# Kernel tuning notes

Measured on AMD Instinct MI355X. Metric: run time of the kernel, lower is better.

The kernel has to match this reference:

```python
import jax, jax.numpy as jnp
import numpy as np

N = 1_000_000
H, W = 480, 640
MIN_DEPTH, MAX_DEPTH = 0.0, 30.0


def setup_inputs() -> dict:
    key = jax.random.key(0)
    k1, k2, k3 = jax.random.split(key, 3)
    scale = jnp.array([W - 1, H - 1], dtype=jnp.float32)
    mkpts0_f = jax.random.uniform(k1, (N, 2), dtype=jnp.float32) * scale
    mkpts1_f = jax.random.uniform(k2, (N, 2), dtype=jnp.float32) * scale
    mconf = jax.random.uniform(k3, (N,), dtype=jnp.float32)
    K = jnp.array([[520.0, 0.0, 320.0],
                   [0.0, 520.0, 240.0],
                   [0.0, 0.0, 1.0]], dtype=jnp.float32)
    K0 = K[None]  # [1,3,3]
    K1 = K[None]
    c, s = float(np.cos(0.1)), float(np.sin(0.1))
    T_0to1 = jnp.array([[c, 0.0, s, 0.2],
                        [0.0, 1.0, 0.0, 0.0],
                        [-s, 0.0, c, 0.05],
                        [0.0, 0.0, 0.0, 1.0]], dtype=jnp.float32)[None]  # [1,4,4]
    image0 = jnp.zeros((1, 1, H, W), dtype=jnp.float32)
    m_bids = jnp.zeros((N,), dtype=jnp.int32)  # single batch element
    return {"T_0to1": T_0to1, "K0": K0, "K1": K1, "mconf": mconf,
            "mkpts0_f": mkpts0_f, "mkpts1_f": mkpts1_f,
            "image0": image0, "m_bids": m_bids}


def _triangulate(T_0to1, K0, K1, mconf, kpts0, kpts1):
    # Projection matrices: P0 = K0 @ [I|0], P1 = K1 @ T[:3,:]
    proj_identity = jnp.eye(3, 4, dtype=K0.dtype)
    P0 = K0[0] @ proj_identity          # [3,4]
    P1 = K1[0] @ T_0to1[0, :3, :]       # [3,4]
    P = jnp.stack([P0, P1], axis=0)     # [V=2,3,4]

    pts = jnp.stack([kpts0, kpts1], axis=1)              # [N,2,2]
    conf = jnp.stack([jnp.ones_like(mconf), mconf], 1)   # [N,2] (self conf = 1)

    # A[n,v] = pts[n,v,:,None] * P[v,2,None,:] - P[v,:2]   -> [N,V,2,4]
    A = pts[..., None] * P[None, :, 2, None, :] - P[None, :, :2, :]
    A = A * conf[:, :, None, None]
    A = A.reshape(A.shape[0], 4, 4)                       # [N,4,4]

    # torch.svd returns V with A = U S V^T; jnp gives Vh = V^T.
    _, _, Vh = jnp.linalg.svd(A)
    v = -Vh[:, 3, :]                                      # [N,4] = -V[:,:,3]
    points_3d = v[:, :3] / v[:, 3:4]                      # homogeneous -> euclidean
    # torch clamps to [-1000,1000] only when infs appear; the final depth value
    # after [0,30] clamp + filter is identical either way, so clip unconditionally.
    points_3d = jnp.clip(points_3d, -1000.0, 1000.0)

    z = jnp.clip(points_3d[:, 2], MIN_DEPTH, MAX_DEPTH)
    filt = (z > MIN_DEPTH) & (z < MAX_DEPTH)
    kp3d_val = z * filt.astype(z.dtype)
    return kp3d_val, points_3d


def reference(T_0to1, K0, K1, mconf, mkpts0_f, mkpts1_f, image0, m_bids):
    h, w = image0.shape[-2], image0.shape[-1]
    kp3d_val, _ = _triangulate(T_0to1, K0, K1, mconf, mkpts0_f, mkpts1_f)
    # generate_sparse_depth: depth[0, y, x] = kp3d_val (long() truncation)
    xi = mkpts0_f[:, 0].astype(jnp.int32)
    yi = mkpts0_f[:, 1].astype(jnp.int32)
    depth0_sparse = jnp.zeros((1, h, w), dtype=kp3d_val.dtype).at[0, yi, xi].set(kp3d_val)
    return depth0_sparse, kp3d_val
```

## Files before the change

kernel.cpp:

```cpp
#include <hip/hip_runtime.h>
#include <math.h>

#define N_PTS 1000000
#define H_IMG 480
#define W_IMG 640
#define PIX (H_IMG * W_IMG)
#define TPB 256
#define BPTS 1024
#define NBLK ((N_PTS + BPTS - 1) / BPTS)


#define ROT64(p, q)                                                            \
  do {                                                                         \
    double apq = Mv[p][q];                                                     \
    if (apq != 0.0) {                                                          \
      double app = Mv[p][p], aqq = Mv[q][q];                                   \
      double d = aqq - app;                                                    \
      double r = sqrt(fma(d, d, 4.0 * apq * apq));                             \
      double t = (2.0 * apq) / (d + copysign(r, d));                           \
      double c = rsqrt(fma(t, t, 1.0));                                        \
      double s = t * c;                                                        \
      Mv[p][p] = fma(-t, apq, app);                                            \
      Mv[q][q] = fma(t, apq, aqq);                                             \
      Mv[p][q] = 0.0;                                                          \
      Mv[q][p] = 0.0;                                                          \
      _Pragma("unroll") for (int k = 0; k < 4; k++) {                          \
        if (k != p && k != q) {                                                \
          double akp = Mv[k][p], akq = Mv[k][q];                               \
          double nkp = c * akp - s * akq;                                      \
          double nkq = s * akp + c * akq;                                      \
          Mv[k][p] = nkp; Mv[p][k] = nkp;                                      \
          Mv[k][q] = nkq; Mv[q][k] = nkq;                                      \
        }                                                                      \
      }                                                                        \
      { double v2p = Vr2[p], v2q = Vr2[q];                                     \
        Vr2[p] = c * v2p - s * v2q; Vr2[q] = s * v2p + c * v2q; }              \
      { double v3p = Vr3[p], v3q = Vr3[q];                                     \
        Vr3[p] = c * v3p - s * v3q; Vr3[q] = s * v3p + c * v3q; }              \
    }                                                                          \
  } while (0)

__device__ float tri_point_fp64(int n,
                                const float* __restrict__ T,
                                const float* __restrict__ K0,
                                const float* __restrict__ K1,
                                const float* __restrict__ mconf,
                                const float* __restrict__ kp0,
                                const float* __restrict__ kp1) {
  float2 p0 = ((const float2*)kp0)[n];
  float2 p1 = ((const float2*)kp1)[n];
  double conf = (double)mconf[n];
  double x0 = (double)p0.x, y0 = (double)p0.y;
  double x1 = (double)p1.x, y1 = (double)p1.y;

  double P0[3][4];
#pragma unroll
  for (int i = 0; i < 3; i++) {
#pragma unroll
    for (int j = 0; j < 3; j++) P0[i][j] = (double)K0[i * 3 + j];
    P0[i][3] = 0.0;
  }
  double P1[3][4];
#pragma unroll
  for (int i = 0; i < 3; i++) {
#pragma unroll
    for (int j = 0; j < 4; j++) {
      double s = 0.0;
#pragma unroll
      for (int k = 0; k < 3; k++)
        s += (double)K1[i * 3 + k] * (double)T[k * 4 + j];
      P1[i][j] = s;
    }
  }

  double Mv[4][4];
#pragma unroll
  for (int i = 0; i < 4; i++)
#pragma unroll
    for (int j = 0; j < 4; j++) Mv[i][j] = 0.0;

  double a[4];
#pragma unroll
  for (int j = 0; j < 4; j++) a[j] = x0 * P0[2][j] - P0[0][j];
#pragma unroll
  for (int i = 0; i < 4; i++)
#pragma unroll
    for (int j = 0; j < 4; j++) Mv[i][j] = fma(a[i], a[j], Mv[i][j]);
#pragma unroll
  for (int j = 0; j < 4; j++) a[j] = y0 * P0[2][j] - P0[1][j];
#pragma unroll
  for (int i = 0; i < 4; i++)
#pragma unroll
    for (int j = 0; j < 4; j++) Mv[i][j] = fma(a[i], a[j], Mv[i][j]);
#pragma unroll
  for (int j = 0; j < 4; j++) a[j] = conf * (x1 * P1[2][j] - P1[0][j]);
#pragma unroll
  for (int i = 0; i < 4; i++)
#pragma unroll
    for (int j = 0; j < 4; j++) Mv[i][j] = fma(a[i], a[j], Mv[i][j]);
#pragma unroll
  for (int j = 0; j < 4; j++) a[j] = conf * (y1 * P1[2][j] - P1[1][j]);
#pragma unroll
  for (int i = 0; i < 4; i++)
#pragma unroll
    for (int j = 0; j < 4; j++) Mv[i][j] = fma(a[i], a[j], Mv[i][j]);

  double Vr2[4] = {0.0, 0.0, 1.0, 0.0};
  double Vr3[4] = {0.0, 0.0, 0.0, 1.0};

  for (int sweep = 0; sweep < 4; sweep++) {
    ROT64(0, 1); ROT64(0, 2); ROT64(0, 3);
    ROT64(1, 2); ROT64(1, 3); ROT64(2, 3);
  }

  double e0 = Mv[0][0], e1 = Mv[1][1], e2 = Mv[2][2], e3 = Mv[3][3];
  bool b01 = e1 < e0;
  double ea = b01 ? e1 : e0;
  double za = b01 ? Vr2[1] : Vr2[0];
  double wa = b01 ? Vr3[1] : Vr3[0];
  bool b23 = e3 < e2;
  double eb = b23 ? e3 : e2;
  double zb = b23 ? Vr2[3] : Vr2[2];
  double wb = b23 ? Vr3[3] : Vr3[2];
  bool bf = eb < ea;
  double vz = bf ? zb : za;
  double vw = bf ? wb : wa;

  double z = vz / vw;
  z = fmin(fmax(z, 0.0), 30.0);
  bool filt = (z > 0.0) && (z < 30.0);
  return filt ? (float)z : 0.0f;
}

#define ROTF_NOV(p, q)                                                         \
  do {                                                                         \
    float apq = Mv[p][q];                                                      \
    if (apq != 0.0f) {                                                         \
      float app = Mv[p][p], aqq = Mv[q][q];                                    \
      float d = aqq - app;                                                     \
      float r = sqrtf(fmaf(d, d, 4.0f * apq * apq));                           \
      float t = __fdividef(2.0f * apq, d + copysignf(r, d));                   \
      float c = rsqrtf(fmaf(t, t, 1.0f));                                      \
      float s = t * c;                                                         \
      Mv[p][p] = fmaf(-t, apq, app);                                           \
      Mv[q][q] = fmaf(t, apq, aqq);                                           \
      Mv[p][q] = 0.0f;                                                         \
      Mv[q][p] = 0.0f;                                                         \
      _Pragma("unroll") for (int k = 0; k < 4; k++) {                          \
        if (k != p && k != q) {                                                \
          float akp = Mv[k][p], akq = Mv[k][q];                                \
          float nkp = c * akp - s * akq;                                       \
          float nkq = s * akp + c * akq;                                       \
          Mv[k][p] = nkp; Mv[p][k] = nkp;                                      \
          Mv[k][q] = nkq; Mv[q][k] = nkq;                                      \
        }                                                                      \
      }                                                                        \
    }                                                                          \
  } while (0)

__global__ __launch_bounds__(TPB) void tri_main(
    const float* __restrict__ T,
    const float* __restrict__ K0,
    const float* __restrict__ K1,
    const float* __restrict__ mconf,
    const float* __restrict__ kp0,
    const float* __restrict__ kp1,
    float* __restrict__ out_kp3d,
    unsigned long long* __restrict__ ws_pix)
{
  __shared__ unsigned short s_list[BPTS];
  __shared__ int s_cnt;

  int tid = threadIdx.x;
  int base = blockIdx.x * BPTS;
  if (tid == 0) s_cnt = 0;
  __syncthreads();

  float P0f[3][4], P1f[3][4];
  double P0d[3][4], P1d[3][4];
#pragma unroll
  for (int i = 0; i < 3; i++) {
#pragma unroll
    for (int j = 0; j < 3; j++) {
      P0f[i][j] = K0[i * 3 + j];
      P0d[i][j] = (double)K0[i * 3 + j];
    }
    P0f[i][3] = 0.0f; P0d[i][3] = 0.0;
  }
#pragma unroll
  for (int i = 0; i < 3; i++) {
#pragma unroll
    for (int j = 0; j < 4; j++) {
      double s = 0.0;
#pragma unroll
      for (int k = 0; k < 3; k++)
        s += (double)K1[i * 3 + k] * (double)T[k * 4 + j];
      P1d[i][j] = s;
      P1f[i][j] = (float)s;
    }
  }

#pragma unroll 1
  for (int r = 0; r < BPTS / TPB; r++) {
    int local = r * TPB + tid;
    int n = base + local;
    if (n >= N_PTS) break;

    float2 p0 = ((const float2*)kp0)[n];
    float2 p1 = ((const float2*)kp1)[n];
    float conff = mconf[n];

    float Mv[4][4];
#pragma unroll
    for (int i = 0; i < 4; i++)
#pragma unroll
      for (int j = 0; j < 4; j++) Mv[i][j] = 0.0f;
    {
      float af[4];
#pragma unroll
      for (int j = 0; j < 4; j++) af[j] = p0.x * P0f[2][j] - P0f[0][j];
#pragma unroll
      for (int i = 0; i < 4; i++)
#pragma unroll
        for (int j = 0; j < 4; j++) Mv[i][j] = fmaf(af[i], af[j], Mv[i][j]);
#pragma unroll
      for (int j = 0; j < 4; j++) af[j] = p0.y * P0f[2][j] - P0f[1][j];
#pragma unroll
      for (int i = 0; i < 4; i++)
#pragma unroll
        for (int j = 0; j < 4; j++) Mv[i][j] = fmaf(af[i], af[j], Mv[i][j]);
#pragma unroll
      for (int j = 0; j < 4; j++)
        af[j] = conff * (p1.x * P1f[2][j] - P1f[0][j]);
#pragma unroll
      for (int i = 0; i < 4; i++)
#pragma unroll
        for (int j = 0; j < 4; j++) Mv[i][j] = fmaf(af[i], af[j], Mv[i][j]);
#pragma unroll
      for (int j = 0; j < 4; j++)
        af[j] = conff * (p1.y * P1f[2][j] - P1f[1][j]);
#pragma unroll
      for (int i = 0; i < 4; i++)
#pragma unroll
        for (int j = 0; j < 4; j++) Mv[i][j] = fmaf(af[i], af[j], Mv[i][j]);
    }

    for (int sweep = 0; sweep < 4; sweep++) {
      ROTF_NOV(0, 1); ROTF_NOV(0, 2); ROTF_NOV(0, 3);
      ROTF_NOV(1, 2); ROTF_NOV(1, 3); ROTF_NOV(2, 3);
    }

    float e0 = Mv[0][0], e1 = Mv[1][1], e2 = Mv[2][2], e3 = Mv[3][3];
    float lo01 = fminf(e0, e1), hi01 = fmaxf(e0, e1);
    float lo23 = fminf(e2, e3), hi23 = fmaxf(e2, e3);
    float emin = fminf(lo01, lo23);
    float esec = fminf(fmaxf(lo01, lo23), fminf(hi01, hi23));
    float trace = e0 + e1 + e2 + e3;
    float g = (esec - emin) / fmaxf(trace, 1e-30f);

    double m00, m01, m02, m03, m11, m12, m13, m22, m23, m33;
    m00 = m01 = m02 = m03 = m11 = m12 = m13 = m22 = m23 = m33 = 0.0;
    {
      double x0 = (double)p0.x, y0 = (double)p0.y;
      double x1 = (double)p1.x, y1 = (double)p1.y;
      double cf = (double)conff;
      double a[4];
#pragma unroll
      for (int rr = 0; rr < 4; rr++) {
        if (rr == 0) {
#pragma unroll
          for (int j = 0; j < 4; j++) a[j] = fma(x0, P0d[2][j], -P0d[0][j]);
        } else if (rr == 1) {
#pragma unroll
          for (int j = 0; j < 4; j++) a[j] = fma(y0, P0d[2][j], -P0d[1][j]);
        } else if (rr == 2) {
#pragma unroll
          for (int j = 0; j < 4; j++)
            a[j] = cf * fma(x1, P1d[2][j], -P1d[0][j]);
        } else {
#pragma unroll
          for (int j = 0; j < 4; j++)
            a[j] = cf * fma(y1, P1d[2][j], -P1d[1][j]);
        }
        m00 = fma(a[0], a[0], m00); m01 = fma(a[0], a[1], m01);
        m02 = fma(a[0], a[2], m02); m03 = fma(a[0], a[3], m03);
        m11 = fma(a[1], a[1], m11); m12 = fma(a[1], a[2], m12);
        m13 = fma(a[1], a[3], m13); m22 = fma(a[2], a[2], m22);
        m23 = fma(a[2], a[3], m23); m33 = fma(a[3], a[3], m33);
      }
    }

    double mu = (double)emin;
    double b00 = m00 - mu, b11 = m11 - mu, b22 = m22 - mu, b33 = m33 - mu;
    double b01 = m01, b02 = m02, b03 = m03, b12 = m12, b13 = m13, b23 = m23;

    double s0 = fma(b00, b11, -b01 * b01);
    double s1 = fma(b00, b12, -b02 * b01);
    double s2 = fma(b00, b13, -b03 * b01);
    double s3 = fma(b01, b12, -b02 * b11);
    double s4 = fma(b01, b13, -b03 * b11);
    double c0 = fma(b02, b13, -b12 * b03);
    double c1 = fma(b02, b23, -b22 * b03);
    double c2 = fma(b02, b33, -b23 * b03);
    double c3 = fma(b12, b23, -b22 * b13);
    double c4 = fma(b12, b33, -b23 * b13);
    double c5 = fma(b22, b33, -b23 * b23);

    double a00 = fma(b11, c5, fma(-b12, c4, b13 * c3));
    double a01 = -fma(b01, c5, fma(-b02, c4, b03 * c3));
    double a11 = fma(b00, c5, fma(-b02, c2, b03 * c1));
    double a02 = fma(b01, c4, fma(-b11, c2, b13 * c0));
    double a12 = -fma(b00, c4, fma(-b01, c2, b03 * c0));
    double a22 = fma(b03, s4, fma(-b13, s2, b33 * s0));
    double a03 = -fma(b01, c3, fma(-b11, c1, b12 * c0));
    double a13 = fma(b00, c3, fma(-b01, c1, b02 * c0));
    double a23 = -fma(b03, s3, fma(-b13, s1, b23 * s0));
    double a33 = fma(b02, s3, fma(-b12, s1, b22 * s0));

    double w10 = a00, w11 = a01, w12 = a02, w13 = a03;
    double bd = fabs(a00);
    { double d1 = fabs(a11);
      bool c = d1 > bd;
      w10 = c ? a01 : w10; w11 = c ? a11 : w11;
      w12 = c ? a12 : w12; w13 = c ? a13 : w13; bd = c ? d1 : bd; }
    { double d2 = fabs(a22);
      bool c = d2 > bd;
      w10 = c ? a02 : w10; w11 = c ? a12 : w11;
      w12 = c ? a22 : w12; w13 = c ? a23 : w13; bd = c ? d2 : bd; }
    { double d3 = fabs(a33);
      bool c = d3 > bd;
      w10 = c ? a03 : w10; w11 = c ? a13 : w11;
      w12 = c ? a23 : w12; w13 = c ? a33 : w13; }

    double w0 = fma(a00, w10, fma(a01, w11, fma(a02, w12, a03 * w13)));
    double w1 = fma(a01, w10, fma(a11, w11, fma(a12, w12, a13 * w13)));
    double w2 = fma(a02, w10, fma(a12, w11, fma(a22, w12, a23 * w13)));
    double w3 = fma(a03, w10, fma(a13, w11, fma(a23, w12, a33 * w13)));

    double inv3 = 1.0 / w3;
    double z = w2 * inv3;

    double wn = fmax(fmax(fabs(w0), fabs(w1)), fmax(fabs(w2), fabs(w3)));
    double gd = (double)fmaxf(g, 1e-30f);
    double theta = 5e-13 / (gd * gd);
    double err_z = theta * wn * (fabs(w2) + fabs(w3)) * (inv3 * inv3);
    err_z = fabs(err_z);

    bool bad = (g < 1e-5f) || !isfinite(z) ||
               (err_z > 0.3) || (fabs(z - 30.0) < err_z);

    if (!bad) {
      double zc = fmin(fmax(z, 0.0), 30.0);
      bool filt = (zc > 0.0) && (zc < 30.0);
      float kp = filt ? (float)zc : 0.0f;
      out_kp3d[n] = kp;
      int pix = (int)p0.y * W_IMG + (int)p0.x;
      atomicMax(&ws_pix[pix],
                ((unsigned long long)(0xC0000000u | (unsigned)n) << 32) |
                    (unsigned long long)__float_as_uint(kp));
    } else {
      int idx = atomicAdd(&s_cnt, 1);
      s_list[idx] = (unsigned short)local;
    }
  }

  __syncthreads();

  int cnt = s_cnt;
  for (int i = tid; i < cnt; i += TPB) {
    int n = base + (int)s_list[i];
    float kp = tri_point_fp64(n, T, K0, K1, mconf, kp0, kp1);
    out_kp3d[n] = kp;
    float2 p0 = ((const float2*)kp0)[n];
    int pix = (int)p0.y * W_IMG + (int)p0.x;
    atomicMax(&ws_pix[pix],
              ((unsigned long long)(0xC0000000u | (unsigned)n) << 32) |
                  (unsigned long long)__float_as_uint(kp));
  }
}

__global__ __launch_bounds__(TPB) void unpack_depth(
    const unsigned long long* __restrict__ ws_pix,
    float* __restrict__ out_depth)
{
  int p = blockIdx.x * blockDim.x + threadIdx.x;
  if (p < PIX) {
    unsigned long long v = ws_pix[p];
    unsigned int hi = (unsigned int)(v >> 32);
    out_depth[p] =
        (hi >= 0xC0000000u) ? __uint_as_float((unsigned int)v) : 0.0f;
  }
}

extern "C" void kernel_launch(void* const* d_in, const int* in_sizes, int n_in,
                              void* d_out, int out_size, void* d_ws, size_t ws_size,
                              hipStream_t stream) {
  const float* T     = (const float*)d_in[0];
  const float* K0    = (const float*)d_in[1];
  const float* K1    = (const float*)d_in[2];
  const float* mconf = (const float*)d_in[3];
  const float* kp0   = (const float*)d_in[4];
  const float* kp1   = (const float*)d_in[5];

  float* out = (float*)d_out;
  unsigned long long* ws_pix = (unsigned long long*)d_ws;

  tri_main<<<NBLK, TPB, 0, stream>>>(T, K0, K1, mconf, kp0, kp1,
                                     out + PIX, ws_pix);

  unpack_depth<<<(PIX + TPB - 1) / TPB, TPB, 0, stream>>>(ws_pix, out);
}
```

Baseline: 140.3 us.

## Replace float Jacobi eigensolve with characteristic-polynomial Laguerre root and power-iteration check

```diff
diff --git a/kernel.cpp b/kernel.cpp
--- a/kernel.cpp
+++ b/kernel.cpp
@@ -132,32 +132,6 @@
   return filt ? (float)z : 0.0f;
 }
 
-#define ROTF_NOV(p, q)                                                         \
-  do {                                                                         \
-    float apq = Mv[p][q];                                                      \
-    if (apq != 0.0f) {                                                         \
-      float app = Mv[p][p], aqq = Mv[q][q];                                    \
-      float d = aqq - app;                                                     \
-      float r = sqrtf(fmaf(d, d, 4.0f * apq * apq));                           \
-      float t = __fdividef(2.0f * apq, d + copysignf(r, d));                   \
-      float c = rsqrtf(fmaf(t, t, 1.0f));                                      \
-      float s = t * c;                                                         \
-      Mv[p][p] = fmaf(-t, apq, app);                                           \
-      Mv[q][q] = fmaf(t, apq, aqq);                                           \
-      Mv[p][q] = 0.0f;                                                         \
-      Mv[q][p] = 0.0f;                                                         \
-      _Pragma("unroll") for (int k = 0; k < 4; k++) {                          \
-        if (k != p && k != q) {                                                \
-          float akp = Mv[k][p], akq = Mv[k][q];                                \
-          float nkp = c * akp - s * akq;                                       \
-          float nkq = s * akp + c * akq;                                       \
-          Mv[k][p] = nkp; Mv[p][k] = nkp;                                      \
-          Mv[k][q] = nkq; Mv[q][k] = nkq;                                      \
-        }                                                                      \
-      }                                                                        \
-    }                                                                          \
-  } while (0)
-
 __global__ __launch_bounds__(TPB) void tri_main(
     const float* __restrict__ T,
     const float* __restrict__ K0,
@@ -176,16 +150,12 @@
   if (tid == 0) s_cnt = 0;
   __syncthreads();
 
-  float P0f[3][4], P1f[3][4];
   double P0d[3][4], P1d[3][4];
 #pragma unroll
   for (int i = 0; i < 3; i++) {
 #pragma unroll
-    for (int j = 0; j < 3; j++) {
-      P0f[i][j] = K0[i * 3 + j];
-      P0d[i][j] = (double)K0[i * 3 + j];
-    }
-    P0f[i][3] = 0.0f; P0d[i][3] = 0.0;
+    for (int j = 0; j < 3; j++) P0d[i][j] = (double)K0[i * 3 + j];
+    P0d[i][3] = 0.0;
   }
 #pragma unroll
   for (int i = 0; i < 3; i++) {
@@ -196,7 +166,6 @@
       for (int k = 0; k < 3; k++)
         s += (double)K1[i * 3 + k] * (double)T[k * 4 + j];
       P1d[i][j] = s;
-      P1f[i][j] = (float)s;
     }
   }
 
@@ -209,54 +178,6 @@
     float2 p0 = ((const float2*)kp0)[n];
     float2 p1 = ((const float2*)kp1)[n];
     float conff = mconf[n];
-
-    float Mv[4][4];
-#pragma unroll
-    for (int i = 0; i < 4; i++)
-#pragma unroll
-      for (int j = 0; j < 4; j++) Mv[i][j] = 0.0f;
-    {
-      float af[4];
-#pragma unroll
-      for (int j = 0; j < 4; j++) af[j] = p0.x * P0f[2][j] - P0f[0][j];
-#pragma unroll
-      for (int i = 0; i < 4; i++)
-#pragma unroll
-        for (int j = 0; j < 4; j++) Mv[i][j] = fmaf(af[i], af[j], Mv[i][j]);
-#pragma unroll
-      for (int j = 0; j < 4; j++) af[j] = p0.y * P0f[2][j] - P0f[1][j];
-#pragma unroll
-      for (int i = 0; i < 4; i++)
-#pragma unroll
-        for (int j = 0; j < 4; j++) Mv[i][j] = fmaf(af[i], af[j], Mv[i][j]);
-#pragma unroll
-      for (int j = 0; j < 4; j++)
-        af[j] = conff * (p1.x * P1f[2][j] - P1f[0][j]);
-#pragma unroll
-      for (int i = 0; i < 4; i++)
-#pragma unroll
-        for (int j = 0; j < 4; j++) Mv[i][j] = fmaf(af[i], af[j], Mv[i][j]);
-#pragma unroll
-      for (int j = 0; j < 4; j++)
-        af[j] = conff * (p1.y * P1f[2][j] - P1f[1][j]);
-#pragma unroll
-      for (int i = 0; i < 4; i++)
-#pragma unroll
-        for (int j = 0; j < 4; j++) Mv[i][j] = fmaf(af[i], af[j], Mv[i][j]);
-    }
-
-    for (int sweep = 0; sweep < 4; sweep++) {
-      ROTF_NOV(0, 1); ROTF_NOV(0, 2); ROTF_NOV(0, 3);
-      ROTF_NOV(1, 2); ROTF_NOV(1, 3); ROTF_NOV(2, 3);
-    }
-
-    float e0 = Mv[0][0], e1 = Mv[1][1], e2 = Mv[2][2], e3 = Mv[3][3];
-    float lo01 = fminf(e0, e1), hi01 = fmaxf(e0, e1);
-    float lo23 = fminf(e2, e3), hi23 = fmaxf(e2, e3);
-    float emin = fminf(lo01, lo23);
-    float esec = fminf(fmaxf(lo01, lo23), fminf(hi01, hi23));
-    float trace = e0 + e1 + e2 + e3;
-    float g = (esec - emin) / fmaxf(trace, 1e-30f);
 
     double m00, m01, m02, m03, m11, m12, m13, m22, m23, m33;
     m00 = m01 = m02 = m03 = m11 = m12 = m13 = m22 = m23 = m33 = 0.0;
@@ -290,32 +211,69 @@
       }
     }
 
-    double mu = (double)emin;
+    double t1 = (m00 + m11) + (m22 + m33);
+    double ms0 = fma(m00, m11, -m01 * m01);
+    double ms1 = fma(m00, m12, -m02 * m01);
+    double ms2 = fma(m00, m13, -m03 * m01);
+    double ms3 = fma(m01, m12, -m02 * m11);
+    double ms4 = fma(m01, m13, -m03 * m11);
+    double mc0 = fma(m02, m13, -m12 * m03);
+    double mc1 = fma(m02, m23, -m22 * m03);
+    double mc2 = fma(m02, m33, -m23 * m03);
+    double mc3 = fma(m12, m23, -m22 * m13);
+    double mc4 = fma(m12, m33, -m23 * m13);
+    double mc5 = fma(m22, m33, -m23 * m23);
+    double A00 = fma(m11, mc5, fma(-m12, mc4, m13 * mc3));
+    double A01 = -fma(m01, mc5, fma(-m02, mc4, m03 * mc3));
+    double A11 = fma(m00, mc5, fma(-m02, mc2, m03 * mc1));
+    double A02 = fma(m01, mc4, fma(-m11, mc2, m13 * mc0));
+    double A03 = -fma(m01, mc3, fma(-m11, mc1, m12 * mc0));
+    double A22 = fma(m03, ms4, fma(-m13, ms2, m33 * ms0));
+    double A33 = fma(m02, ms3, fma(-m12, ms1, m22 * ms0));
+    double t3 = (A00 + A11) + (A22 + A33);
+    double t4 = fma(m00, A00, fma(m01, A01, fma(m02, A02, m03 * A03)));
+    double q02 = fma(m00, m22, -m02 * m02);
+    double q03 = fma(m00, m33, -m03 * m03);
+    double q12 = fma(m11, m22, -m12 * m12);
+    double q13 = fma(m11, m33, -m13 * m13);
+    double t2 = ((ms0 + mc5) + (q02 + q03)) + (q12 + q13);
+
+    double mu = t4 / t3;
+    double t1_3 = 3.0 * t1, t1_6 = 6.0 * t1, t2_2 = 2.0 * t2;
+#pragma unroll
+    for (int it = 0; it < 3; it++) {
+      double pv = fma(fma(fma(mu - t1, mu, t2), mu, -t3), mu, t4);
+      double pd = fma(fma(fma(4.0, mu, -t1_3), mu, t2_2), mu, -t3);
+      double pdd = fma(fma(12.0, mu, -t1_6), mu, t2_2);
+      double rad = 3.0 * fma(3.0 * pd, pd, -4.0 * pv * pdd);
+      double sq = sqrt(fmax(rad, 0.0));
+      double den = pd + copysign(sq, pd);
+      mu = mu - 4.0 * pv / den;
+    }
+
     double b00 = m00 - mu, b11 = m11 - mu, b22 = m22 - mu, b33 = m33 - mu;
-    double b01 = m01, b02 = m02, b03 = m03, b12 = m12, b13 = m13, b23 = m23;
-
-    double s0 = fma(b00, b11, -b01 * b01);
-    double s1 = fma(b00, b12, -b02 * b01);
-    double s2 = fma(b00, b13, -b03 * b01);
-    double s3 = fma(b01, b12, -b02 * b11);
-    double s4 = fma(b01, b13, -b03 * b11);
-    double c0 = fma(b02, b13, -b12 * b03);
-    double c1 = fma(b02, b23, -b22 * b03);
-    double c2 = fma(b02, b33, -b23 * b03);
-    double c3 = fma(b12, b23, -b22 * b13);
-    double c4 = fma(b12, b33, -b23 * b13);
-    double c5 = fma(b22, b33, -b23 * b23);
-
-    double a00 = fma(b11, c5, fma(-b12, c4, b13 * c3));
-    double a01 = -fma(b01, c5, fma(-b02, c4, b03 * c3));
-    double a11 = fma(b00, c5, fma(-b02, c2, b03 * c1));
-    double a02 = fma(b01, c4, fma(-b11, c2, b13 * c0));
-    double a12 = -fma(b00, c4, fma(-b01, c2, b03 * c0));
-    double a22 = fma(b03, s4, fma(-b13, s2, b33 * s0));
-    double a03 = -fma(b01, c3, fma(-b11, c1, b12 * c0));
-    double a13 = fma(b00, c3, fma(-b01, c1, b02 * c0));
-    double a23 = -fma(b03, s3, fma(-b13, s1, b23 * s0));
-    double a33 = fma(b02, s3, fma(-b12, s1, b22 * s0));
+    double s0 = fma(b00, b11, -m01 * m01);
+    double s1 = fma(b00, m12, -m02 * m01);
+    double s2 = fma(b00, m13, -m03 * m01);
+    double s3 = fma(m01, m12, -m02 * b11);
+    double s4 = fma(m01, m13, -m03 * b11);
+    double c0 = fma(m02, m13, -m12 * m03);
+    double c1 = fma(m02, m23, -b22 * m03);
+    double c2 = fma(m02, b33, -m23 * m03);
+    double c3 = fma(m12, m23, -b22 * m13);
+    double c4 = fma(m12, b33, -m23 * m13);
+    double c5 = fma(b22, b33, -m23 * m23);
+
+    double a00 = fma(b11, c5, fma(-m12, c4, m13 * c3));
+    double a01 = -fma(m01, c5, fma(-m02, c4, m03 * c3));
+    double a11 = fma(b00, c5, fma(-m02, c2, m03 * c1));
+    double a02 = fma(m01, c4, fma(-b11, c2, m13 * c0));
+    double a12 = -fma(b00, c4, fma(-m01, c2, m03 * c0));
+    double a22 = fma(m03, s4, fma(-m13, s2, b33 * s0));
+    double a03 = -fma(m01, c3, fma(-b11, c1, m12 * c0));
+    double a13 = fma(b00, c3, fma(-m01, c1, m02 * c0));
+    double a23 = -fma(m03, s3, fma(-m13, s1, m23 * s0));
+    double a33 = fma(m02, s3, fma(-m12, s1, b22 * s0));
 
     double w10 = a00, w11 = a01, w12 = a02, w13 = a03;
     double bd = fabs(a00);
@@ -332,25 +290,21 @@
       w10 = c ? a03 : w10; w11 = c ? a13 : w11;
       w12 = c ? a23 : w12; w13 = c ? a33 : w13; }
 
-    double w0 = fma(a00, w10, fma(a01, w11, fma(a02, w12, a03 * w13)));
-    double w1 = fma(a01, w10, fma(a11, w11, fma(a12, w12, a13 * w13)));
-    double w2 = fma(a02, w10, fma(a12, w11, fma(a22, w12, a23 * w13)));
-    double w3 = fma(a03, w10, fma(a13, w11, fma(a23, w12, a33 * w13)));
-
-    double inv3 = 1.0 / w3;
-    double z = w2 * inv3;
-
-    double wn = fmax(fmax(fabs(w0), fabs(w1)), fmax(fabs(w2), fabs(w3)));
-    double gd = (double)fmaxf(g, 1e-30f);
-    double theta = 5e-13 / (gd * gd);
-    double err_z = theta * wn * (fabs(w2) + fabs(w3)) * (inv3 * inv3);
-    err_z = fabs(err_z);
-
-    bool bad = (g < 1e-5f) || !isfinite(z) ||
-               (err_z > 0.3) || (fabs(z - 30.0) < err_z);
-
-    if (!bad) {
-      double zc = fmin(fmax(z, 0.0), 30.0);
+    double u0 = fma(a00, w10, fma(a01, w11, fma(a02, w12, a03 * w13)));
+    double u1 = fma(a01, w10, fma(a11, w11, fma(a12, w12, a13 * w13)));
+    double u2 = fma(a02, w10, fma(a12, w11, fma(a22, w12, a23 * w13)));
+    double u3 = fma(a03, w10, fma(a13, w11, fma(a23, w12, a33 * w13)));
+    double v2 = fma(a02, u0, fma(a12, u1, fma(a22, u2, a23 * u3)));
+    double v3 = fma(a03, u0, fma(a13, u1, fma(a23, u2, a33 * u3)));
+
+    double z2 = u2 / u3;
+    double z3 = v2 / v3;
+
+    double tol = 1e-3 * fmax(1.0, fabs(z3));
+    bool ok = (fabs(z3 - z2) < tol) && (fabs(z3 - 30.0) > 0.1);
+
+    if (ok) {
+      double zc = fmin(fmax(z3, 0.0), 30.0);
       bool filt = (zc > 0.0) && (zc < 30.0);
       float kp = filt ? (float)zc : 0.0f;
       out_kp3d[n] = kp;
```

After: 126.1 us. 10.1% less time.
